# Kernel tuning notes

Measured on AMD Instinct MI355X. Metric: run time of the kernel, lower is better.

## Reference

```python
import jax, jax.numpy as jnp
from jax import lax
import numpy as np

# dims
B, C, H, W, T = 8, 2, 64, 64, 200
# per-layer neuron configs (defaults from NetworkBasic.__init__)
THETA = (30.0, 50.0, 100.0)
TAU_SR = (1.0, 2.0, 4.0)
TAU_REF = (1.0, 2.0, 4.0)
SCALE_REF = (1.0, 1.0, 1.0)
TAU_RHO = (1.0, 1.0, 10.0)


def psp(x, tau):
    """SLAYER synaptic response: first-order leaky integration over time axis (last).
    a[t] = exp(-1/tau) * a[t-1] + x[t]"""
    d = jnp.exp(jnp.asarray(-1.0 / tau, x.dtype))
    xt = jnp.moveaxis(x, -1, 0)  # [T, B, C, H, W]
    def step(a, xi):
        a = d * a + xi
        return a, a
    _, ys = lax.scan(step, jnp.zeros_like(xt[0]), xt)
    return jnp.moveaxis(ys, 0, -1)


def spike(u, theta, tau_ref, scale_ref, tau_rho):
    """SLAYER spiking unit: threshold + leaky refractory state, sequential over T.
    Forward emits hard spikes; surrogate (sigmoid) used only for gradients."""
    dref = jnp.exp(jnp.asarray(-1.0 / tau_ref, u.dtype))
    th = jnp.asarray(theta, u.dtype)
    ut = jnp.moveaxis(u, -1, 0)  # [T, ...]
    def step(r, ui):
        v = ui + r
        hard = (v >= th).astype(u.dtype)
        sur = jax.nn.sigmoid((v - th) / tau_rho)
        s = sur + lax.stop_gradient(hard - sur)  # straight-through surrogate
        r2 = dref * r - th * scale_ref * s       # refractory subtraction
        return r2, s
    _, s = lax.scan(step, jnp.zeros_like(ut[0]), ut)
    return jnp.moveaxis(s, 0, -1)


def conv2d_t(x, w, pad):
    """slayer.conv: spatial conv applied independently per timestep (kernel kxkx1, no bias)."""
    Bb, Cc, Hh, Ww, Tt = x.shape
    xt = jnp.moveaxis(x, -1, 1).reshape(Bb * Tt, Cc, Hh, Ww)
    y = lax.conv_general_dilated(xt, w, (1, 1), [(pad, pad), (pad, pad)],
                                 dimension_numbers=("NCHW", "OIHW", "NCHW"))
    O = w.shape[0]
    return jnp.moveaxis(y.reshape(Bb, Tt, O, Hh, Ww), 1, -1)


def convT2d_t(x, w):
    """slayer.convTranspose kernel=2 stride=2, per timestep (exact 2x upsample)."""
    Bb, Cc, Hh, Ww, Tt = x.shape
    xt = jnp.moveaxis(x, -1, 1).reshape(Bb * Tt, Cc, Hh, Ww)
    y = lax.conv_transpose(xt, w, (2, 2), "VALID",
                           dimension_numbers=("NCHW", "OIHW", "NCHW"))
    O = w.shape[0]
    return jnp.moveaxis(y.reshape(Bb, Tt, O, 2 * Hh, 2 * Ww), 1, -1)


def setup_inputs() -> dict:
    key = jax.random.key(0)
    k0, k1, k2, k3 = jax.random.split(key, 4)
    spikeInput = (jax.random.uniform(k0, (B, C, H, W, T)) < 0.3).astype(jnp.float32)
    w1 = jax.random.normal(k1, (8, 2, 5, 5), jnp.float32) * 10.0
    w2 = jax.random.normal(k2, (8, 8, 3, 3), jnp.float32) * 10.0
    wup = jax.random.normal(k3, (2, 8, 2, 2), jnp.float32) * 10.0
    return {"spikeInput": spikeInput, "w1": w1, "w2": w2, "wup": wup}


def reference(spikeInput, w1, w2, wup):
    Bb, Cc, Hh, Ww, Tt = spikeInput.shape
    psp1 = psp(spikeInput, TAU_SR[0])
    psp1_up = jax.image.resize(psp1, (Bb, Cc, 2 * Hh, 2 * Ww, Tt), method="linear")
    s1 = spike(conv2d_t(psp1, w1, 2), THETA[0], TAU_REF[0], SCALE_REF[0], TAU_RHO[0])
    s2 = spike(conv2d_t(psp(s1, TAU_SR[1]), w2, 1), THETA[1], TAU_REF[1], SCALE_REF[1], TAU_RHO[1])
    s3 = spike(convT2d_t(psp(s2, TAU_SR[2]), wup) + psp1_up,
               THETA[2], TAU_REF[2], SCALE_REF[2], TAU_RHO[2])
    return s3
```

## Files before the change

### kernel.cpp

```cpp
#include <hip/hip_runtime.h>

#define DEC1 0.36787944117144233f
#define DEC2 0.60653065971263342f
#define DEC3 0.77880078307140487f

__global__ void prep_weights(const float* __restrict__ w1,
                             const float* __restrict__ w2,
                             const float* __restrict__ wup,
                             float* __restrict__ wr)
{
    int i = blockIdx.x * 256 + threadIdx.x;
    if (i < 400) {
        int o = i & 7, tap = i >> 3;
        int c = tap / 25, rem = tap % 25, ky = rem / 5, kx = rem % 5;
        wr[i] = w1[((o * 2 + c) * 5 + ky) * 5 + kx];
    }
    if (i < 576) {
        int o = i & 7, tap = i >> 3;
        int c = tap / 9, rem = tap % 9, ky = rem / 3, kx = rem % 3;
        wr[400 + i] = w2[((o * 8 + c) * 3 + ky) * 3 + kx];
    }
    if (i < 64) {
        int c = i & 7, r = i >> 3;
        int dj = r & 1, di = (r >> 1) & 1, o = r >> 2;
        wr[976 + i] = wup[((o * 8 + c) * 2 + (1 - di)) * 2 + (1 - dj)];
    }
}

static __device__ __forceinline__ float4 spike_psp4(float4 u, float th, float dref,
                                                    float dq, float& r, float& q)
{
    float4 qv; float v, s;
    v = __fadd_rn(u.x, r); s = (v >= th) ? 1.f : 0.f;
    r = __fsub_rn(__fmul_rn(dref, r), __fmul_rn(th, s));
    q = __fadd_rn(__fmul_rn(dq, q), s); qv.x = q;
    v = __fadd_rn(u.y, r); s = (v >= th) ? 1.f : 0.f;
    r = __fsub_rn(__fmul_rn(dref, r), __fmul_rn(th, s));
    q = __fadd_rn(__fmul_rn(dq, q), s); qv.y = q;
    v = __fadd_rn(u.z, r); s = (v >= th) ? 1.f : 0.f;
    r = __fsub_rn(__fmul_rn(dref, r), __fmul_rn(th, s));
    q = __fadd_rn(__fmul_rn(dq, q), s); qv.z = q;
    v = __fadd_rn(u.w, r); s = (v >= th) ? 1.f : 0.f;
    r = __fsub_rn(__fmul_rn(dref, r), __fmul_rn(th, s));
    q = __fadd_rn(__fmul_rn(dq, q), s); qv.w = q;
    return qv;
}

static __device__ __forceinline__ float4 spike4(float4 u, float th, float dref, float& r)
{
    float4 ov; float v, s;
    v = __fadd_rn(u.x, r); s = (v >= th) ? 1.f : 0.f;
    r = __fsub_rn(__fmul_rn(dref, r), __fmul_rn(th, s)); ov.x = s;
    v = __fadd_rn(u.y, r); s = (v >= th) ? 1.f : 0.f;
    r = __fsub_rn(__fmul_rn(dref, r), __fmul_rn(th, s)); ov.y = s;
    v = __fadd_rn(u.z, r); s = (v >= th) ? 1.f : 0.f;
    r = __fsub_rn(__fmul_rn(dref, r), __fmul_rn(th, s)); ov.z = s;
    v = __fadd_rn(u.w, r); s = (v >= th) ? 1.f : 0.f;
    r = __fsub_rn(__fmul_rn(dref, r), __fmul_rn(th, s)); ov.w = s;
    return ov;
}

#define FMA4(ACC_, W_, D_) { ACC_.x += (W_)*(D_).x; ACC_.y += (W_)*(D_).y; \
                             ACC_.z += (W_)*(D_).z; ACC_.w += (W_)*(D_).w; }

#define PSP4(V_, X_, st) { \
    V_.x = __fadd_rn(__fmul_rn(DEC1, st),   X_.x); \
    V_.y = __fadd_rn(__fmul_rn(DEC1, V_.x), X_.y); \
    V_.z = __fadd_rn(__fmul_rn(DEC1, V_.y), X_.z); \
    V_.w = __fadd_rn(__fmul_rn(DEC1, V_.z), X_.w); st = V_.w; }

__global__ __launch_bounds__(256, 2)
void snn_fused(const float* __restrict__ spk,
               const float* __restrict__ wr,
               float* __restrict__ out)
{
    const int tid  = threadIdx.x;
    const int b    = blockIdx.x >> 6;
    const int tile = blockIdx.x & 63;
    const int gy0  = (tile >> 3) << 3;
    const int gx0  = (tile & 7) << 3;

    __shared__ float4 sP1[2][2][2][196];
    __shared__ float4 sP2[8][2][100];
    __shared__ float4 sP3[8][2][64];

    float aP0 = 0.f, aP1 = 0.f;
    float rB[4], qB[4], rC[4], qC[4], r3[4];
#pragma unroll
    for (int i = 0; i < 4; ++i) { rB[i]=0.f; qB[i]=0.f; rC[i]=0.f; qC[i]=0.f; r3[i]=0.f; }

    const int ary = tid / 14, arx = tid % 14;
    const int aiy = gy0 - 3 + ary, aix = gx0 - 3 + arx;
    const bool avalid = (tid < 196) && (aiy >= 0) && (aiy < 64) && (aix >= 0) && (aix < 64);
    const int aoff0 = avalid ? (((b * 2 + 0) * 64 + aiy) * 64 + aix) * 200 : 0;
    const int aoff1 = avalid ? (((b * 2 + 1) * 64 + aiy) * 64 + aix) * 200 : 0;

    const int ochB = __builtin_amdgcn_readfirstlane(tid >> 7);
    const int bpx  = tid & 127;
    const int by   = bpx / 10, bx = bpx % 10;

    const int ochC = __builtin_amdgcn_readfirstlane(tid >> 6) & 1;
    const int cpx  = tid & 63;
    const int cy   = cpx >> 3, cx = cpx & 7;

    const int od   = __builtin_amdgcn_readfirstlane(tid >> 6);
    const int dy   = cpx >> 3, dxx = cpx & 7;
    const int diy  = gy0 + dy, dix = gx0 + dxx;

    const float wy0_0 = (diy == 0)  ? 0.f : 0.25f;
    const float wy1_0 = (diy == 0)  ? 1.f : 0.75f;
    const float wy0_1 = (diy == 63) ? 1.f : 0.75f;
    const float wy1_1 = (diy == 63) ? 0.f : 0.25f;
    const float wx0_0 = (dix == 0)  ? 0.f : 0.25f;
    const float wx1_0 = (dix == 0)  ? 1.f : 0.75f;
    const float wx0_1 = (dix == 63) ? 1.f : 0.75f;
    const float wx1_1 = (dix == 63) ? 0.f : 0.25f;

    float4 x00 = make_float4(0.f,0.f,0.f,0.f), x01 = x00, x10 = x00, x11 = x00;
    if (avalid) {
        x00 = *(const float4*)(spk + aoff0);
        x01 = *(const float4*)(spk + aoff0 + 4);
        x10 = *(const float4*)(spk + aoff1);
        x11 = *(const float4*)(spk + aoff1 + 4);
    }

#pragma unroll 1
    for (int ck = 0; ck < 25; ++ck) {
        const int t0 = ck * 8;
        const int p  = ck & 1;

        if (tid < 196) {
            float4 v;
            PSP4(v, x00, aP0); sP1[p][0][0][tid] = v;
            PSP4(v, x01, aP0); sP1[p][0][1][tid] = v;
            PSP4(v, x10, aP1); sP1[p][1][0][tid] = v;
            PSP4(v, x11, aP1); sP1[p][1][1][tid] = v;
            if (ck < 24 && avalid) {
                x00 = *(const float4*)(spk + aoff0 + t0 + 8);
                x01 = *(const float4*)(spk + aoff0 + t0 + 12);
                x10 = *(const float4*)(spk + aoff1 + t0 + 8);
                x11 = *(const float4*)(spk + aoff1 + t0 + 12);
            }
        }
        __syncthreads();

        if (bpx < 100) {
            float4 a0[4], a1[4];
#pragma unroll
            for (int j = 0; j < 4; ++j) { a0[j] = make_float4(0.f,0.f,0.f,0.f); a1[j] = a0[j]; }
            const float* wB = wr + ochB * 4;
#pragma unroll 1
            for (int c = 0; c < 2; ++c) {
#pragma unroll 1
                for (int ky = 0; ky < 5; ++ky) {
                    const float4* r0 = &sP1[p][c][0][(by + ky) * 14 + bx];
                    const float4* r1 = &sP1[p][c][1][(by + ky) * 14 + bx];
                    const float*  wrow = wB + (c * 25 + ky * 5) * 8;
#pragma unroll
                    for (int kx = 0; kx < 5; ++kx) {
                        float4 d0 = r0[kx], d1 = r1[kx];
#pragma unroll
                        for (int j = 0; j < 4; ++j) {
                            float wv = wrow[kx * 8 + j];
                            FMA4(a0[j], wv, d0); FMA4(a1[j], wv, d1);
                        }
                    }
                }
            }
#pragma unroll
            for (int j = 0; j < 4; ++j) {
                float4 q0 = spike_psp4(a0[j], 30.f, DEC1, DEC2, rB[j], qB[j]);
                sP2[ochB * 4 + j][0][bpx] = q0;
                float4 q1 = spike_psp4(a1[j], 30.f, DEC1, DEC2, rB[j], qB[j]);
                sP2[ochB * 4 + j][1][bpx] = q1;
            }
        }
        __syncthreads();

        if (tid < 128) {
            float4 a0[4], a1[4];
#pragma unroll
            for (int j = 0; j < 4; ++j) { a0[j] = make_float4(0.f,0.f,0.f,0.f); a1[j] = a0[j]; }
            const float* wC = wr + 400 + ochC * 4;
#pragma unroll 1
            for (int c = 0; c < 8; ++c) {
#pragma unroll 1
                for (int ky = 0; ky < 3; ++ky) {
                    const float4* r0 = &sP2[c][0][(cy + ky) * 10 + cx];
                    const float4* r1 = &sP2[c][1][(cy + ky) * 10 + cx];
                    const float*  wrow = wC + (c * 9 + ky * 3) * 8;
#pragma unroll
                    for (int kx = 0; kx < 3; ++kx) {
                        float4 d0 = r0[kx], d1 = r1[kx];
#pragma unroll
                        for (int j = 0; j < 4; ++j) {
                            float wv = wrow[kx * 8 + j];
                            FMA4(a0[j], wv, d0); FMA4(a1[j], wv, d1);
                        }
                    }
                }
            }
#pragma unroll
            for (int j = 0; j < 4; ++j) {
                float4 q0 = spike_psp4(a0[j], 50.f, DEC2, DEC3, rC[j], qC[j]);
                sP3[ochC * 4 + j][0][cpx] = q0;
                float4 q1 = spike_psp4(a1[j], 50.f, DEC2, DEC3, rC[j], qC[j]);
                sP3[ochC * 4 + j][1][cpx] = q1;
            }
        }
        __syncthreads();

        if (tid < 128) {
#pragma unroll 1
            for (int h = 0; h < 2; ++h) {
                float4 p3[8];
#pragma unroll
                for (int c = 0; c < 8; ++c) p3[c] = sP3[c][h][cpx];
                float4 P[3][3];
#pragma unroll
                for (int sy = 0; sy < 3; ++sy)
#pragma unroll
                for (int sx = 0; sx < 3; ++sx)
                    P[sy][sx] = sP1[p][od][h][(dy + 2 + sy) * 14 + (dxx + 2 + sx)];

#pragma unroll
                for (int di = 0; di < 2; ++di) {
                    const float ay  = di ? wy0_1 : wy0_0;
                    const float byw = di ? wy1_1 : wy1_0;
#pragma unroll
                    for (int dj = 0; dj < 2; ++dj) {
                        const float ax  = dj ? wx0_1 : wx0_0;
                        const float bxw = dj ? wx1_1 : wx1_0;
                        float4 tv = make_float4(0.f, 0.f, 0.f, 0.f);
                        const float* wD = wr + 976 + ((od * 2 + di) * 2 + dj) * 8;
#pragma unroll
                        for (int c = 0; c < 8; ++c) {
                            float wv = wD[c];
                            FMA4(tv, wv, p3[c]);
                        }
                        float4 A = P[di][dj],      Bv = P[di][dj + 1];
                        float4 Cv = P[di + 1][dj], Dv = P[di + 1][dj + 1];
                        float4 up, u; float ra, rb;
                        ra = __fadd_rn(__fmul_rn(ay, A.x),  __fmul_rn(byw, Cv.x));
                        rb = __fadd_rn(__fmul_rn(ay, Bv.x), __fmul_rn(byw, Dv.x));
                        up.x = __fadd_rn(__fmul_rn(ax, ra), __fmul_rn(bxw, rb));
                        ra = __fadd_rn(__fmul_rn(ay, A.y),  __fmul_rn(byw, Cv.y));
                        rb = __fadd_rn(__fmul_rn(ay, Bv.y), __fmul_rn(byw, Dv.y));
                        up.y = __fadd_rn(__fmul_rn(ax, ra), __fmul_rn(bxw, rb));
                        ra = __fadd_rn(__fmul_rn(ay, A.z),  __fmul_rn(byw, Cv.z));
                        rb = __fadd_rn(__fmul_rn(ay, Bv.z), __fmul_rn(byw, Dv.z));
                        up.z = __fadd_rn(__fmul_rn(ax, ra), __fmul_rn(bxw, rb));
                        ra = __fadd_rn(__fmul_rn(ay, A.w),  __fmul_rn(byw, Cv.w));
                        rb = __fadd_rn(__fmul_rn(ay, Bv.w), __fmul_rn(byw, Dv.w));
                        up.w = __fadd_rn(__fmul_rn(ax, ra), __fmul_rn(bxw, rb));
                        u.x = __fadd_rn(tv.x, up.x);
                        u.y = __fadd_rn(tv.y, up.y);
                        u.z = __fadd_rn(tv.z, up.z);
                        u.w = __fadd_rn(tv.w, up.w);
                        const int sub = di * 2 + dj;
                        float4 ov = spike4(u, 100.f, DEC3, r3[sub]);
                        float* op = out + ((((b * 2 + od) * 128 + (2 * diy + di)) * 128)
                                           + (2 * dix + dj)) * 200 + t0 + h * 4;
                        *(float4*)op = ov;
                    }
                }
            }
        }
    }
}

extern "C" void kernel_launch(void* const* d_in, const int* in_sizes, int n_in,
                              void* d_out, int out_size, void* d_ws, size_t ws_size,
                              hipStream_t stream)
{
    const float* spk = (const float*)d_in[0];
    const float* w1  = (const float*)d_in[1];
    const float* w2  = (const float*)d_in[2];
    const float* wup = (const float*)d_in[3];
    float* outp = (float*)d_out;
    float* wr   = (float*)d_ws;

    prep_weights<<<dim3(3), dim3(256), 0, stream>>>(w1, w2, wup, wr);
    snn_fused<<<dim3(512), dim3(256), 0, stream>>>(spk, wr, outp);
}
```

Measured before the change: 654.1 us.

## Spread stage-C and output stage across all four waves, pad shared rows to 16

Stage C (3x3 conv) now runs on all 256 threads, each computing 2 output channels instead of 4 on 128 threads, and the output/upsample stage splits the vertical sub-pixel index across waves so every thread handles half the work. The sP1 row stride is padded from 14 to 16, and stage-B pixels are remapped so the first 80 lanes cover whole 8-wide rows, which changes the LDS access pattern. The intent is to remove idle half-block phases and shorten the serial critical path per chunk, at the cost of more LDS space and a little extra index arithmetic.

```diff
diff --git a/kernel.cpp b/kernel.cpp
--- a/kernel.cpp
+++ b/kernel.cpp
@@ -80,16 +80,19 @@
     const int gy0  = (tile >> 3) << 3;
     const int gx0  = (tile & 7) << 3;
 
-    __shared__ float4 sP1[2][2][2][196];
+    __shared__ float4 sP1[2][2][2][224];
     __shared__ float4 sP2[8][2][100];
     __shared__ float4 sP3[8][2][64];
 
     float aP0 = 0.f, aP1 = 0.f;
-    float rB[4], qB[4], rC[4], qC[4], r3[4];
-#pragma unroll
-    for (int i = 0; i < 4; ++i) { rB[i]=0.f; qB[i]=0.f; rC[i]=0.f; qC[i]=0.f; r3[i]=0.f; }
+    float rB[4], qB[4];
+    float rC[2] = {0.f, 0.f}, qC[2] = {0.f, 0.f};
+    float r3[2] = {0.f, 0.f};
+#pragma unroll
+    for (int i = 0; i < 4; ++i) { rB[i] = 0.f; qB[i] = 0.f; }
 
     const int ary = tid / 14, arx = tid % 14;
+    const int aidx = ary * 16 + arx;
     const int aiy = gy0 - 3 + ary, aix = gx0 - 3 + arx;
     const bool avalid = (tid < 196) && (aiy >= 0) && (aiy < 64) && (aix >= 0) && (aix < 64);
     const int aoff0 = avalid ? (((b * 2 + 0) * 64 + aiy) * 64 + aix) * 200 : 0;
@@ -97,24 +100,30 @@
 
     const int ochB = __builtin_amdgcn_readfirstlane(tid >> 7);
     const int bpx  = tid & 127;
-    const int by   = bpx / 10, bx = bpx % 10;
-
-    const int ochC = __builtin_amdgcn_readfirstlane(tid >> 6) & 1;
+    int by_, bx_;
+    if (bpx < 80) { by_ = bpx >> 3; bx_ = bpx & 7; }
+    else          { int t2 = bpx - 80; by_ = t2 >> 1; bx_ = 8 + (t2 & 1); }
+    const int by = by_, bx = bx_;
+    const int bwr = by * 10 + bx;
+
+    const int wvC  = __builtin_amdgcn_readfirstlane(tid >> 6);
+    const int ochC = wvC * 2;
     const int cpx  = tid & 63;
     const int cy   = cpx >> 3, cx = cpx & 7;
 
-    const int od   = __builtin_amdgcn_readfirstlane(tid >> 6);
-    const int dy   = cpx >> 3, dxx = cpx & 7;
-    const int diy  = gy0 + dy, dix = gx0 + dxx;
-
-    const float wy0_0 = (diy == 0)  ? 0.f : 0.25f;
-    const float wy1_0 = (diy == 0)  ? 1.f : 0.75f;
-    const float wy0_1 = (diy == 63) ? 1.f : 0.75f;
-    const float wy1_1 = (diy == 63) ? 0.f : 0.25f;
-    const float wx0_0 = (dix == 0)  ? 0.f : 0.25f;
-    const float wx1_0 = (dix == 0)  ? 1.f : 0.75f;
-    const float wx0_1 = (dix == 63) ? 1.f : 0.75f;
-    const float wx1_1 = (dix == 63) ? 0.f : 0.25f;
+    const int od  = tid >> 7;
+    const int ddi = (tid >> 6) & 1;
+    const int dpx = tid & 63;
+    const int dy  = dpx >> 3, dxx = dpx & 7;
+    const int diy = gy0 + dy, dix = gx0 + dxx;
+
+    const float ay  = ddi ? ((diy == 63) ? 1.f : 0.75f) : ((diy == 0) ? 0.f : 0.25f);
+    const float byw = ddi ? ((diy == 63) ? 0.f : 0.25f) : ((diy == 0) ? 1.f : 0.75f);
+    const float ax0 = (dix == 0)  ? 0.f : 0.25f;
+    const float bx0 = (dix == 0)  ? 1.f : 0.75f;
+    const float ax1 = (dix == 63) ? 1.f : 0.75f;
+    const float bx1 = (dix == 63) ? 0.f : 0.25f;
+    const int   didx = (dy + 2 + ddi) * 16 + (dxx + 2);
 
     float4 x00 = make_float4(0.f,0.f,0.f,0.f), x01 = x00, x10 = x00, x11 = x00;
     if (avalid) {
@@ -131,10 +140,10 @@
 
         if (tid < 196) {
             float4 v;
-            PSP4(v, x00, aP0); sP1[p][0][0][tid] = v;
-            PSP4(v, x01, aP0); sP1[p][0][1][tid] = v;
-            PSP4(v, x10, aP1); sP1[p][1][0][tid] = v;
-            PSP4(v, x11, aP1); sP1[p][1][1][tid] = v;
+            PSP4(v, x00, aP0); sP1[p][0][0][aidx] = v;
+            PSP4(v, x01, aP0); sP1[p][0][1][aidx] = v;
+            PSP4(v, x10, aP1); sP1[p][1][0][aidx] = v;
+            PSP4(v, x11, aP1); sP1[p][1][1][aidx] = v;
             if (ck < 24 && avalid) {
                 x00 = *(const float4*)(spk + aoff0 + t0 + 8);
                 x01 = *(const float4*)(spk + aoff0 + t0 + 12);
@@ -153,8 +162,8 @@
             for (int c = 0; c < 2; ++c) {
 #pragma unroll 1
                 for (int ky = 0; ky < 5; ++ky) {
-                    const float4* r0 = &sP1[p][c][0][(by + ky) * 14 + bx];
-                    const float4* r1 = &sP1[p][c][1][(by + ky) * 14 + bx];
+                    const float4* r0 = &sP1[p][c][0][(by + ky) * 16 + bx];
+                    const float4* r1 = &sP1[p][c][1][(by + ky) * 16 + bx];
                     const float*  wrow = wB + (c * 25 + ky * 5) * 8;
 #pragma unroll
                     for (int kx = 0; kx < 5; ++kx) {
@@ -170,18 +179,16 @@
 #pragma unroll
             for (int j = 0; j < 4; ++j) {
                 float4 q0 = spike_psp4(a0[j], 30.f, DEC1, DEC2, rB[j], qB[j]);
-                sP2[ochB * 4 + j][0][bpx] = q0;
+                sP2[ochB * 4 + j][0][bwr] = q0;
                 float4 q1 = spike_psp4(a1[j], 30.f, DEC1, DEC2, rB[j], qB[j]);
-                sP2[ochB * 4 + j][1][bpx] = q1;
+                sP2[ochB * 4 + j][1][bwr] = q1;
             }
         }
         __syncthreads();
 
-        if (tid < 128) {
-            float4 a0[4], a1[4];
-#pragma unroll
-            for (int j = 0; j < 4; ++j) { a0[j] = make_float4(0.f,0.f,0.f,0.f); a1[j] = a0[j]; }
-            const float* wC = wr + 400 + ochC * 4;
+        {
+            float4 a00 = make_float4(0.f,0.f,0.f,0.f), a01 = a00, a10 = a00, a11 = a00;
+            const float* wC = wr + 400 + ochC;
 #pragma unroll 1
             for (int c = 0; c < 8; ++c) {
 #pragma unroll 1
@@ -192,77 +199,68 @@
 #pragma unroll
                     for (int kx = 0; kx < 3; ++kx) {
                         float4 d0 = r0[kx], d1 = r1[kx];
-#pragma unroll
-                        for (int j = 0; j < 4; ++j) {
-                            float wv = wrow[kx * 8 + j];
-                            FMA4(a0[j], wv, d0); FMA4(a1[j], wv, d1);
-                        }
+                        float w0 = wrow[kx * 8], w1 = wrow[kx * 8 + 1];
+                        FMA4(a00, w0, d0); FMA4(a01, w0, d1);
+                        FMA4(a10, w1, d0); FMA4(a11, w1, d1);
                     }
                 }
             }
-#pragma unroll
-            for (int j = 0; j < 4; ++j) {
-                float4 q0 = spike_psp4(a0[j], 50.f, DEC2, DEC3, rC[j], qC[j]);
-                sP3[ochC * 4 + j][0][cpx] = q0;
-                float4 q1 = spike_psp4(a1[j], 50.f, DEC2, DEC3, rC[j], qC[j]);
-                sP3[ochC * 4 + j][1][cpx] = q1;
-            }
+            float4 qv;
+            qv = spike_psp4(a00, 50.f, DEC2, DEC3, rC[0], qC[0]); sP3[ochC][0][cpx] = qv;
+            qv = spike_psp4(a01, 50.f, DEC2, DEC3, rC[0], qC[0]); sP3[ochC][1][cpx] = qv;
+            qv = spike_psp4(a10, 50.f, DEC2, DEC3, rC[1], qC[1]); sP3[ochC + 1][0][cpx] = qv;
+            qv = spike_psp4(a11, 50.f, DEC2, DEC3, rC[1], qC[1]); sP3[ochC + 1][1][cpx] = qv;
         }
         __syncthreads();
 
-        if (tid < 128) {
+        {
 #pragma unroll 1
             for (int h = 0; h < 2; ++h) {
                 float4 p3[8];
 #pragma unroll
-                for (int c = 0; c < 8; ++c) p3[c] = sP3[c][h][cpx];
-                float4 P[3][3];
-#pragma unroll
-                for (int sy = 0; sy < 3; ++sy)
-#pragma unroll
-                for (int sx = 0; sx < 3; ++sx)
-                    P[sy][sx] = sP1[p][od][h][(dy + 2 + sy) * 14 + (dxx + 2 + sx)];
-
-#pragma unroll
-                for (int di = 0; di < 2; ++di) {
-                    const float ay  = di ? wy0_1 : wy0_0;
-                    const float byw = di ? wy1_1 : wy1_0;
-#pragma unroll
-                    for (int dj = 0; dj < 2; ++dj) {
-                        const float ax  = dj ? wx0_1 : wx0_0;
-                        const float bxw = dj ? wx1_1 : wx1_0;
-                        float4 tv = make_float4(0.f, 0.f, 0.f, 0.f);
-                        const float* wD = wr + 976 + ((od * 2 + di) * 2 + dj) * 8;
-#pragma unroll
-                        for (int c = 0; c < 8; ++c) {
-                            float wv = wD[c];
-                            FMA4(tv, wv, p3[c]);
-                        }
-                        float4 A = P[di][dj],      Bv = P[di][dj + 1];
-                        float4 Cv = P[di + 1][dj], Dv = P[di + 1][dj + 1];
-                        float4 up, u; float ra, rb;
-                        ra = __fadd_rn(__fmul_rn(ay, A.x),  __fmul_rn(byw, Cv.x));
-                        rb = __fadd_rn(__fmul_rn(ay, Bv.x), __fmul_rn(byw, Dv.x));
-                        up.x = __fadd_rn(__fmul_rn(ax, ra), __fmul_rn(bxw, rb));
-                        ra = __fadd_rn(__fmul_rn(ay, A.y),  __fmul_rn(byw, Cv.y));
-                        rb = __fadd_rn(__fmul_rn(ay, Bv.y), __fmul_rn(byw, Dv.y));
-                        up.y = __fadd_rn(__fmul_rn(ax, ra), __fmul_rn(bxw, rb));
-                        ra = __fadd_rn(__fmul_rn(ay, A.z),  __fmul_rn(byw, Cv.z));
-                        rb = __fadd_rn(__fmul_rn(ay, Bv.z), __fmul_rn(byw, Dv.z));
-                        up.z = __fadd_rn(__fmul_rn(ax, ra), __fmul_rn(bxw, rb));
-                        ra = __fadd_rn(__fmul_rn(ay, A.w),  __fmul_rn(byw, Cv.w));
-                        rb = __fadd_rn(__fmul_rn(ay, Bv.w), __fmul_rn(byw, Dv.w));
-                        up.w = __fadd_rn(__fmul_rn(ax, ra), __fmul_rn(bxw, rb));
-                        u.x = __fadd_rn(tv.x, up.x);
-                        u.y = __fadd_rn(tv.y, up.y);
-                        u.z = __fadd_rn(tv.z, up.z);
-                        u.w = __fadd_rn(tv.w, up.w);
-                        const int sub = di * 2 + dj;
-                        float4 ov = spike4(u, 100.f, DEC3, r3[sub]);
-                        float* op = out + ((((b * 2 + od) * 128 + (2 * diy + di)) * 128)
-                                           + (2 * dix + dj)) * 200 + t0 + h * 4;
-                        *(float4*)op = ov;
+                for (int c = 0; c < 8; ++c) p3[c] = sP3[c][h][dpx];
+                float4 P0a = sP1[p][od][h][didx];
+                float4 P0b = sP1[p][od][h][didx + 1];
+                float4 P0c = sP1[p][od][h][didx + 2];
+                float4 P1a = sP1[p][od][h][didx + 16];
+                float4 P1b = sP1[p][od][h][didx + 17];
+                float4 P1c = sP1[p][od][h][didx + 18];
+#pragma unroll
+                for (int dj = 0; dj < 2; ++dj) {
+                    const float ax  = dj ? ax1 : ax0;
+                    const float bxw = dj ? bx1 : bx0;
+                    float4 tv = make_float4(0.f, 0.f, 0.f, 0.f);
+                    const float* wD = wr + 976 + ((od * 2 + ddi) * 2 + dj) * 8;
+#pragma unroll
+                    for (int c = 0; c < 8; ++c) {
+                        float wv = wD[c];
+                        FMA4(tv, wv, p3[c]);
                     }
+                    float4 A  = dj ? P0b : P0a;
+                    float4 Bv = dj ? P0c : P0b;
+                    float4 Cv = dj ? P1b : P1a;
+                    float4 Dv = dj ? P1c : P1b;
+                    float4 up, u; float ra, rb;
+                    ra = __fadd_rn(__fmul_rn(ay, A.x),  __fmul_rn(byw, Cv.x));
+                    rb = __fadd_rn(__fmul_rn(ay, Bv.x), __fmul_rn(byw, Dv.x));
+                    up.x = __fadd_rn(__fmul_rn(ax, ra), __fmul_rn(bxw, rb));
+                    ra = __fadd_rn(__fmul_rn(ay, A.y),  __fmul_rn(byw, Cv.y));
+                    rb = __fadd_rn(__fmul_rn(ay, Bv.y), __fmul_rn(byw, Dv.y));
+                    up.y = __fadd_rn(__fmul_rn(ax, ra), __fmul_rn(bxw, rb));
+                    ra = __fadd_rn(__fmul_rn(ay, A.z),  __fmul_rn(byw, Cv.z));
+                    rb = __fadd_rn(__fmul_rn(ay, Bv.z), __fmul_rn(byw, Dv.z));
+                    up.z = __fadd_rn(__fmul_rn(ax, ra), __fmul_rn(bxw, rb));
+                    ra = __fadd_rn(__fmul_rn(ay, A.w),  __fmul_rn(byw, Cv.w));
+                    rb = __fadd_rn(__fmul_rn(ay, Bv.w), __fmul_rn(byw, Dv.w));
+                    up.w = __fadd_rn(__fmul_rn(ax, ra), __fmul_rn(bxw, rb));
+                    u.x = __fadd_rn(tv.x, up.x);
+                    u.y = __fadd_rn(tv.y, up.y);
+                    u.z = __fadd_rn(tv.z, up.z);
+                    u.w = __fadd_rn(tv.w, up.w);
+                    float4 ov = spike4(u, 100.f, DEC3, r3[dj]);
+                    float* op = out + ((((b * 2 + od) * 128 + (2 * diy + ddi)) * 128)
+                                       + (2 * dix + dj)) * 200 + t0 + h * 4;
+                    *(float4*)op = ov;
                 }
             }
         }
```

Measured after the change: 603.8 us. 1.08x faster.
